# Optimization experiments

Measured on AMD Instinct MI355X. Metric: run time of the kernel, lower is better.

Reference implementation:

```python
import jax, jax.numpy as jnp
import numpy as np

B, H, W, NF = 2, 80, 80, 128  # batch, height, width, n_filter
CIN = 2 * NF                  # input channels (final conv outputs 2*NF and adds to x)


def _conv(x, w):
    # 3x3, stride 1, SAME, no bias; NHWC / HWIO
    return jax.lax.conv_general_dilated(
        x, w, window_strides=(1, 1), padding='SAME',
        dimension_numbers=('NHWC', 'HWIO', 'NHWC'))


def setup_inputs() -> dict:
    key = jax.random.key(0)
    ks = jax.random.split(key, 5)
    def glorot(k, shape):
        fan_in = shape[0] * shape[1] * shape[2]
        fan_out = shape[0] * shape[1] * shape[3]
        lim = np.sqrt(6.0 / (fan_in + fan_out)).astype(np.float32)
        return jax.random.uniform(k, shape, jnp.float32, -lim, lim)
    return {
        'x': jax.random.normal(ks[0], (B, H, W, CIN), jnp.float32),
        'w_theta': glorot(ks[1], (3, 3, CIN, NF)),
        'w_phi':   glorot(ks[2], (3, 3, CIN, NF)),
        'w_g':     glorot(ks[3], (3, 3, CIN, NF)),
        'w_conv':  glorot(ks[4], (3, 3, NF, CIN)),
    }


def reference(x, w_theta, w_phi, w_g, w_conv):
    b, h, w, cin = x.shape
    c = w_theta.shape[-1]  # n_filter
    n = h * w
    theta = _conv(x, w_theta).reshape(b, n, c)        # (B, N, C)
    # NOTE: Keras Reshape((n_filter,-1)) is a row-major reshape, NOT a transpose
    phi = _conv(x, w_phi).reshape(b, c, n)            # (B, C, N)
    attn = jax.nn.softmax(jnp.einsum('bnc,bcm->bnm', theta, phi), axis=-1)  # (B, N, N)
    g = _conv(x, w_g).reshape(b, n, c)                # (B, N, C)
    out = jnp.einsum('bnm,bmc->bnc', attn, g).reshape(b, h, w, c)
    out = _conv(out, w_conv)                          # (B, H, W, 2C)
    return x + out
```

## Files before the change

### kernel.cpp

```cpp
#include <hip/hip_runtime.h>
#include <hip/hip_bf16.h>

#define HH_ 80
#define WW_ 80
#define CIN_ 256
#define NF_ 128
#define NPIX_ 6400
#define NTOK_ 12800
#define NELEM_ (NTOK_ * NF_)
#define NXEL_  (NTOK_ * CIN_)
#define KW_    2304
#define KWC_   1152
#define WEL_   294912

#define KVS_    8
#define KVB_    32
#define MCHUNK_ 800
#define NIT_    25

__device__ float g_theta[NELEM_];
__device__ float g_phi  [NELEM_];
__device__ float g_gv   [NELEM_];
__device__ unsigned short g_aob[NELEM_];
__device__ unsigned short g_th_hi[NELEM_], g_th_lo[NELEM_];
__device__ unsigned short g_phT_hi[NELEM_], g_phT_lo[NELEM_];
__device__ unsigned short g_gT[NELEM_];
__device__ float g_po [KVS_ * NELEM_];
__device__ float g_pml[KVS_ * NTOK_ * 2];
__device__ unsigned short g_xh[NXEL_], g_xl[NXEL_];
__device__ unsigned short g_wtTh[WEL_], g_wtTl[WEL_];
__device__ unsigned short g_wpTh[WEL_], g_wpTl[WEL_];
__device__ unsigned short g_wgT[WEL_];
__device__ unsigned short g_wcT[WEL_];

__device__ __forceinline__ float b2f(unsigned short u) {
    union { unsigned int i; float f; } v; v.i = ((unsigned int)u) << 16; return v.f;
}
__device__ __forceinline__ unsigned short f2b(float f) {
    union { float f; unsigned int i; } v; v.f = f;
    unsigned int i = v.i;
    i += 0x7fffu + ((i >> 16) & 1u);
    return (unsigned short)(i >> 16);
}

typedef __attribute__((ext_vector_type(8))) short bf16x8;
typedef __attribute__((ext_vector_type(4))) float f32x4;

__device__ __forceinline__ f32x4 mfma16(bf16x8 a, bf16x8 b, f32x4 c) {
    return __builtin_amdgcn_mfma_f32_16x16x32_bf16(a, b, c, 0, 0, 0);
}

__global__ __launch_bounds__(256) void prep_x(const float* __restrict__ x)
{
    const int i = (blockIdx.x * 256 + threadIdx.x) * 4;
    if (i >= NXEL_) return;
    const float4 v = *(const float4*)(x + i);
    ushort4 hi, lo;
    hi.x = f2b(v.x); lo.x = f2b(v.x - b2f(hi.x));
    hi.y = f2b(v.y); lo.y = f2b(v.y - b2f(hi.y));
    hi.z = f2b(v.z); lo.z = f2b(v.z - b2f(hi.z));
    hi.w = f2b(v.w); lo.w = f2b(v.w - b2f(hi.w));
    *(ushort4*)(g_xh + i) = hi;
    *(ushort4*)(g_xl + i) = lo;
}

__global__ __launch_bounds__(256) void prep_w(
    const float* __restrict__ wt, const float* __restrict__ wp,
    const float* __restrict__ wg, const float* __restrict__ wc)
{
    const int i = blockIdx.x * 256 + threadIdx.x;
    if (i >= WEL_) return;
    {
        const int t  = i / (256 * 128);
        const int r  = i % (256 * 128);
        const int ci = r >> 7;
        const int f  = r & 127;
        const size_t d = (size_t)(t * 8 + (ci >> 5)) * 4096
                       + (size_t)f * 32 + (ci & 31);
        const float tv = wt[i];
        const unsigned short th = f2b(tv);
        g_wtTh[d] = th; g_wtTl[d] = f2b(tv - b2f(th));
        const float pv = wp[i];
        const unsigned short ph = f2b(pv);
        g_wpTh[d] = ph; g_wpTl[d] = f2b(pv - b2f(ph));
        g_wgT[d] = f2b(wg[i]);
    }
    {
        const int t  = i / (128 * 256);
        const int r  = i % (128 * 256);
        const int ci = r >> 8;
        const int f  = r & 255;
        const size_t d = (size_t)(t * 4 + (ci >> 5)) * 8192
                       + (size_t)f * 32 + (ci & 31);
        g_wcT[d] = f2b(wc[i]);
    }
}

__global__ __launch_bounds__(512) void conv3_mfma()
{
    __shared__ __align__(16) unsigned short w_lds[5][128][40];
    __shared__ __align__(16) unsigned short x_lds[64][2][40];

    const int tid  = threadIdx.x;
    const int wv   = tid >> 6;
    const int lane = tid & 63;
    const int quad = lane >> 4;
    const int ll   = lane & 15;
    const int wp   = wv >> 2;
    const int wf   = wv & 3;
    const int P0   = blockIdx.x * 64;
    const int fb   = wf * 32;

    const int sxp = tid >> 3;
    const int sxh = (tid >> 2) & 1;
    const int sxc = (tid & 3) * 8;
    const int swf = tid >> 2;
    const int swc = (tid & 3) * 8;

    const int sp  = P0 + sxp;
    const int spb = sp / NPIX_;
    const int spl = sp % NPIX_;
    const int sph = spl / WW_;
    const int spw = spl % WW_;

    const bf16x8 ZV = {0,0,0,0,0,0,0,0};
    bf16x8 rx, rw0, rw1, rw2, rw3, rw4;

#define C3_STAGE_LOAD(s)                                                      \
    {                                                                         \
        const int t_ = (s) >> 3, kc_ = (s) & 7;                               \
        const int hh_ = sph + t_ / 3 - 1, ww_ = spw + t_ % 3 - 1;             \
        if (hh_ >= 0 && hh_ < HH_ && ww_ >= 0 && ww_ < WW_) {                 \
            const size_t src_ = ((size_t)spb * NPIX_ + hh_ * WW_ + ww_) * CIN_\
                                + kc_ * 32 + sxc;                             \
            rx = sxh ? *(const bf16x8*)(g_xl + src_)                          \
                     : *(const bf16x8*)(g_xh + src_);                         \
        } else rx = ZV;                                                       \
        const size_t ws_ = (size_t)(s) * 4096 + (size_t)swf * 32 + swc;       \
        rw0 = *(const bf16x8*)(g_wtTh + ws_);                                 \
        rw1 = *(const bf16x8*)(g_wtTl + ws_);                                 \
        rw2 = *(const bf16x8*)(g_wpTh + ws_);                                 \
        rw3 = *(const bf16x8*)(g_wpTl + ws_);                                 \
        rw4 = *(const bf16x8*)(g_wgT  + ws_);                                 \
    }

#define C3_STAGE_WRITE()                                                      \
    {                                                                         \
        *(bf16x8*)(&x_lds[sxp][sxh][sxc]) = rx;                               \
        *(bf16x8*)(&w_lds[0][swf][swc]) = rw0;                                \
        *(bf16x8*)(&w_lds[1][swf][swc]) = rw1;                                \
        *(bf16x8*)(&w_lds[2][swf][swc]) = rw2;                                \
        *(bf16x8*)(&w_lds[3][swf][swc]) = rw3;                                \
        *(bf16x8*)(&w_lds[4][swf][swc]) = rw4;                                \
    }

    f32x4 aT[2][2], aP[2][2], aG[2][2];
    #pragma unroll
    for (int pt = 0; pt < 2; ++pt)
        #pragma unroll
        for (int ft = 0; ft < 2; ++ft) {
            aT[pt][ft] = (f32x4){0.f,0.f,0.f,0.f};
            aP[pt][ft] = (f32x4){0.f,0.f,0.f,0.f};
            aG[pt][ft] = (f32x4){0.f,0.f,0.f,0.f};
        }

    C3_STAGE_LOAD(0);
    C3_STAGE_WRITE();
    __syncthreads();

    for (int s = 0; s < 72; ++s) {
        const bool pf = (s + 1 < 72);
        if (pf) C3_STAGE_LOAD(s + 1);

        bf16x8 xa[2][2];
        #pragma unroll
        for (int pt = 0; pt < 2; ++pt) {
            const int px = wp * 32 + pt * 16 + ll;
            xa[pt][0] = *(const bf16x8*)(&x_lds[px][0][quad * 8]);
            xa[pt][1] = *(const bf16x8*)(&x_lds[px][1][quad * 8]);
        }
        #pragma unroll
        for (int ft = 0; ft < 2; ++ft) {
            const int f = fb + ft * 16 + ll;
            const bf16x8 tH = *(const bf16x8*)(&w_lds[0][f][quad * 8]);
            const bf16x8 tL = *(const bf16x8*)(&w_lds[1][f][quad * 8]);
            const bf16x8 pH = *(const bf16x8*)(&w_lds[2][f][quad * 8]);
            const bf16x8 pL = *(const bf16x8*)(&w_lds[3][f][quad * 8]);
            const bf16x8 gB = *(const bf16x8*)(&w_lds[4][f][quad * 8]);
            #pragma unroll
            for (int pt = 0; pt < 2; ++pt) {
                aT[pt][ft] = mfma16(xa[pt][0], tH, aT[pt][ft]);
                aT[pt][ft] = mfma16(xa[pt][0], tL, aT[pt][ft]);
                aT[pt][ft] = mfma16(xa[pt][1], tH, aT[pt][ft]);
                aP[pt][ft] = mfma16(xa[pt][0], pH, aP[pt][ft]);
                aP[pt][ft] = mfma16(xa[pt][0], pL, aP[pt][ft]);
                aP[pt][ft] = mfma16(xa[pt][1], pH, aP[pt][ft]);
                aG[pt][ft] = mfma16(xa[pt][0], gB, aG[pt][ft]);
            }
        }

        __syncthreads();
        if (pf) C3_STAGE_WRITE();
        __syncthreads();
    }

    #pragma unroll
    for (int pt = 0; pt < 2; ++pt)
        #pragma unroll
        for (int ft = 0; ft < 2; ++ft) {
            const int f = fb + ft * 16 + ll;
            #pragma unroll
            for (int r = 0; r < 4; ++r) {
                const size_t n = P0 + wp * 32 + pt * 16 + quad * 4 + r;
                g_theta[n * NF_ + f] = aT[pt][ft][r];
                g_phi  [n * NF_ + f] = aP[pt][ft][r];
                g_gv   [n * NF_ + f] = aG[pt][ft][r];
            }
        }
#undef C3_STAGE_LOAD
#undef C3_STAGE_WRITE
}

__global__ __launch_bounds__(256) void prep_pack()
{
    const int i = blockIdx.x * 256 + threadIdx.x;
    if (i >= NELEM_) return;
    const int n  = i >> 7;
    const int c  = i & 127;
    const int b  = n / NPIX_;
    const int nl = n % NPIX_;

    const float tv = g_theta[i];
    const unsigned short th = f2b(tv);
    g_th_hi[i] = th;
    g_th_lo[i] = f2b(tv - b2f(th));

    const float pv = g_phi[i];
    const int j  = nl * 128 + c;
    const int cp = j / NPIX_;
    const int mp = j % NPIX_;
    const unsigned short phh = f2b(pv);
    const size_t o = (size_t)b * (NPIX_ * NF_) + (size_t)mp * 128 + cp;
    g_phT_hi[o] = phh;
    g_phT_lo[o] = f2b(pv - b2f(phh));

    g_gT[(size_t)b * (NPIX_ * NF_) + (size_t)c * NPIX_ + nl] = f2b(g_gv[i]);
}

__global__ __launch_bounds__(256) void attn_mfma()
{
    __shared__ __align__(16) unsigned short kh_lds[KVB_][136];
    __shared__ __align__(16) unsigned short kl_lds[KVB_][136];
    __shared__ __align__(16) unsigned short v_lds[NF_][40];
    __shared__ __align__(16) short p_lds[4][16 * 40];

    const int tid  = threadIdx.x;
    const int w    = tid >> 6;
    const int lane = tid & 63;
    const int quad = lane >> 4;
    const int ll   = lane & 15;

    const int cid = blockIdx.x & 15;
    const int qw  = blockIdx.x >> 4;
    const int b   = cid >> 3;
    const int kvs = cid & 7;
    const int R0  = b * NPIX_ + qw * 64;
    const int m_start = kvs * MCHUNK_;

    const unsigned short* phH = g_phT_hi + (size_t)b * (NPIX_ * NF_);
    const unsigned short* phL = g_phT_lo + (size_t)b * (NPIX_ * NF_);
    const unsigned short* gT  = g_gT    + (size_t)b * (NPIX_ * NF_);

    bf16x8 aH[4], aL[4];
    #pragma unroll
    for (int kk = 0; kk < 4; ++kk) {
        const size_t off = (size_t)(R0 + w * 16 + ll) * 128 + kk * 32 + quad * 8;
        aH[kk] = *(const bf16x8*)(g_th_hi + off);
        aL[kk] = *(const bf16x8*)(g_th_lo + off);
    }

    f32x4 acc[8];
    #pragma unroll
    for (int t = 0; t < 8; ++t) acc[t] = (f32x4){0.f, 0.f, 0.f, 0.f};
    float mi = -1e30f, li = 0.f;

    const int kr0 = tid >> 4;
    const int kc0 = (tid & 15) * 8;
    const int vr0 = tid >> 2;
    const int vm0 = (tid & 3) * 8;

    bf16x8 skh0, skh1, skl0, skl1, sv0, sv1;

    {
        const int m0 = m_start;
        skh0 = *(const bf16x8*)(phH + (size_t)(m0 + kr0) * 128 + kc0);
        skh1 = *(const bf16x8*)(phH + (size_t)(m0 + kr0 + 16) * 128 + kc0);
        skl0 = *(const bf16x8*)(phL + (size_t)(m0 + kr0) * 128 + kc0);
        skl1 = *(const bf16x8*)(phL + (size_t)(m0 + kr0 + 16) * 128 + kc0);
        sv0  = *(const bf16x8*)(gT + (size_t)vr0 * NPIX_ + m0 + vm0);
        sv1  = *(const bf16x8*)(gT + (size_t)(vr0 + 64) * NPIX_ + m0 + vm0);
        *(bf16x8*)(&kh_lds[kr0][kc0])      = skh0;
        *(bf16x8*)(&kh_lds[kr0 + 16][kc0]) = skh1;
        *(bf16x8*)(&kl_lds[kr0][kc0])      = skl0;
        *(bf16x8*)(&kl_lds[kr0 + 16][kc0]) = skl1;
        *(bf16x8*)(&v_lds[vr0][vm0])       = sv0;
        *(bf16x8*)(&v_lds[vr0 + 64][vm0])  = sv1;
    }
    __syncthreads();

    short* pl = &p_lds[w][0];

    for (int it = 0; it < NIT_; ++it) {
        const bool pf = (it + 1 < NIT_);
        if (pf) {
            const int m0 = m_start + (it + 1) * KVB_;
            skh0 = *(const bf16x8*)(phH + (size_t)(m0 + kr0) * 128 + kc0);
            skh1 = *(const bf16x8*)(phH + (size_t)(m0 + kr0 + 16) * 128 + kc0);
            skl0 = *(const bf16x8*)(phL + (size_t)(m0 + kr0) * 128 + kc0);
            skl1 = *(const bf16x8*)(phL + (size_t)(m0 + kr0 + 16) * 128 + kc0);
            sv0  = *(const bf16x8*)(gT + (size_t)vr0 * NPIX_ + m0 + vm0);
            sv1  = *(const bf16x8*)(gT + (size_t)(vr0 + 64) * NPIX_ + m0 + vm0);
        }

        f32x4 s[2];
        #pragma unroll
        for (int mt = 0; mt < 2; ++mt) {
            f32x4 s0 = (f32x4){0.f,0.f,0.f,0.f};
            const int mrow = mt * 16 + ll;
            #pragma unroll
            for (int kk = 0; kk < 4; ++kk) {
                const bf16x8 bH = *(const bf16x8*)(&kh_lds[mrow][kk * 32 + quad * 8]);
                const bf16x8 bL = *(const bf16x8*)(&kl_lds[mrow][kk * 32 + quad * 8]);
                s0 = mfma16(bH, aH[kk], s0);
                s0 = mfma16(bL, aH[kk], s0);
                s0 = mfma16(bH, aL[kk], s0);
            }
            s[mt] = s0;
        }

        float cm = fmaxf(fmaxf(fmaxf(s[0][0], s[0][1]), fmaxf(s[0][2], s[0][3])),
                         fmaxf(fmaxf(s[1][0], s[1][1]), fmaxf(s[1][2], s[1][3])));
        cm = fmaxf(cm, __shfl_xor(cm, 16));
        cm = fmaxf(cm, __shfl_xor(cm, 32));
        const bool nog = __all(cm <= mi + 4.0f);
        if (!nog) {
            const float nm = fmaxf(mi, cm);
            const float al = __expf(mi - nm);
            mi = nm;
            li *= al;
            if (quad == 0)
                ((float*)(pl + (ll >> 2) * 40 + 32))[ll & 3] = al;
        }
        float ssum = 0.f;
        #pragma unroll
        for (int mt = 0; mt < 2; ++mt)
            #pragma unroll
            for (int r = 0; r < 4; ++r) {
                const float e = __expf(s[mt][r] - mi);
                s[mt][r] = e; ssum += e;
            }
        ssum += __shfl_xor(ssum, 16);
        ssum += __shfl_xor(ssum, 32);
        li += ssum;

        #pragma unroll
        for (int mt = 0; mt < 2; ++mt) {
            unsigned int c0_, c1_;
            asm("v_cvt_pk_bf16_f32 %0, %1, %2"
                : "=v"(c0_) : "v"(s[mt][0]), "v"(s[mt][1]));
            asm("v_cvt_pk_bf16_f32 %0, %1, %2"
                : "=v"(c1_) : "v"(s[mt][2]), "v"(s[mt][3]));
            *(uint2*)(pl + ll * 40 + mt * 16 + quad * 4) = make_uint2(c0_, c1_);
        }

        if (!nog) {
            const float* alp = (const float*)(pl + quad * 40 + 32);
            #pragma unroll
            for (int r = 0; r < 4; ++r) {
                const float av = alp[r];
                #pragma unroll
                for (int t = 0; t < 8; ++t) acc[t][r] *= av;
            }
        }

        const bf16x8 pa = *(const bf16x8*)(pl + ll * 40 + quad * 8);

        #pragma unroll
        for (int ct = 0; ct < 8; ++ct) {
            const bf16x8 gb = *(const bf16x8*)(&v_lds[ct * 16 + ll][quad * 8]);
            acc[ct] = mfma16(pa, gb, acc[ct]);
        }

        __syncthreads();
        if (pf) {
            *(bf16x8*)(&kh_lds[kr0][kc0])      = skh0;
            *(bf16x8*)(&kh_lds[kr0 + 16][kc0]) = skh1;
            *(bf16x8*)(&kl_lds[kr0][kc0])      = skl0;
            *(bf16x8*)(&kl_lds[kr0 + 16][kc0]) = skl1;
            *(bf16x8*)(&v_lds[vr0][vm0])       = sv0;
            *(bf16x8*)(&v_lds[vr0 + 64][vm0])  = sv1;
        }
        __syncthreads();
    }

    const int row0 = R0 + w * 16;
    #pragma unroll
    for (int ct = 0; ct < 8; ++ct)
        #pragma unroll
        for (int r = 0; r < 4; ++r)
            g_po[((size_t)kvs * NTOK_ + row0 + quad * 4 + r) * NF_ + ct * 16 + ll]
                = acc[ct][r];
    if (quad == 0) {
        const size_t mlidx = ((size_t)kvs * NTOK_ + row0 + ll) * 2;
        g_pml[mlidx]     = mi;
        g_pml[mlidx + 1] = li;
    }
}

__global__ __launch_bounds__(256) void merge_attn()
{
    const int idx = blockIdx.x * 256 + threadIdx.x;
    const int row = idx >> 4;
    const int c0  = (idx & 15) * 8;

    float m[KVS_], l[KVS_];
    #pragma unroll
    for (int s = 0; s < KVS_; ++s) {
        const size_t mlidx = ((size_t)s * NTOK_ + row) * 2;
        m[s] = g_pml[mlidx];
        l[s] = g_pml[mlidx + 1];
    }
    float M = m[0];
    #pragma unroll
    for (int s = 1; s < KVS_; ++s) M = fmaxf(M, m[s]);
    float a[KVS_], L = 0.f;
    #pragma unroll
    for (int s = 0; s < KVS_; ++s) {
        a[s] = __expf(m[s] - M);
        L += a[s] * l[s];
    }
    const float inv = 1.f / L;

    float o[8];
    #pragma unroll
    for (int j = 0; j < 8; ++j) o[j] = 0.f;
    #pragma unroll
    for (int s = 0; s < KVS_; ++s) {
        const float* p = g_po + ((size_t)s * NTOK_ + row) * NF_ + c0;
        const float4 p0 = *(const float4*)(p);
        const float4 p1 = *(const float4*)(p + 4);
        o[0] += a[s] * p0.x; o[1] += a[s] * p0.y;
        o[2] += a[s] * p0.z; o[3] += a[s] * p0.w;
        o[4] += a[s] * p1.x; o[5] += a[s] * p1.y;
        o[6] += a[s] * p1.z; o[7] += a[s] * p1.w;
    }
    unsigned short tmp[8];
    #pragma unroll
    for (int j = 0; j < 8; ++j) tmp[j] = f2b(o[j] * inv);
    unsigned short* dst = g_aob + (size_t)row * NF_ + c0;
    *(ushort4*)(dst)     = make_ushort4(tmp[0], tmp[1], tmp[2], tmp[3]);
    *(ushort4*)(dst + 4) = make_ushort4(tmp[4], tmp[5], tmp[6], tmp[7]);
}

__global__ __launch_bounds__(512) void conv_out_mfma(
    const float* __restrict__ x, float* __restrict__ out)
{
    __shared__ __align__(16) unsigned short w_lds[256][40];
    __shared__ __align__(16) unsigned short a_lds[64][40];

    const int tid  = threadIdx.x;
    const int wv   = tid >> 6;
    const int lane = tid & 63;
    const int quad = lane >> 4;
    const int ll   = lane & 15;
    const int wp   = wv >> 2;
    const int wf   = wv & 3;
    const int P0   = blockIdx.x * 64;
    const int fb   = wf * 64;

    const int swf = tid >> 1;
    const int swc = (tid & 1) * 16;
    const int sap = tid >> 2;
    const int sac = (tid & 3) * 8;

    const int sp  = P0 + sap;
    const int spb = sp / NPIX_;
    const int spl = sp % NPIX_;
    const int sph = spl / WW_;
    const int spw = spl % WW_;

    const bf16x8 ZV = {0,0,0,0,0,0,0,0};
    bf16x8 ra, rwA, rwB;

#define CO_STAGE_LOAD(s)                                                      \
    {                                                                         \
        const int t_ = (s) >> 2, kc_ = (s) & 3;                               \
        if (tid < 256) {                                                      \
            const int hh_ = sph + t_ / 3 - 1, ww_ = spw + t_ % 3 - 1;         \
            if (hh_ >= 0 && hh_ < HH_ && ww_ >= 0 && ww_ < WW_) {             \
                const size_t src_ = ((size_t)spb * NPIX_ + hh_ * WW_ + ww_)   \
                                    * NF_ + kc_ * 32 + sac;                   \
                ra = *(const bf16x8*)(g_aob + src_);                          \
            } else ra = ZV;                                                   \
        }                                                                     \
        const size_t ws_ = (size_t)(s) * 8192 + (size_t)swf * 32 + swc;       \
        rwA = *(const bf16x8*)(g_wcT + ws_);                                  \
        rwB = *(const bf16x8*)(g_wcT + ws_ + 8);                              \
    }

#define CO_STAGE_WRITE()                                                      \
    {                                                                         \
        if (tid < 256) *(bf16x8*)(&a_lds[sap][sac]) = ra;                     \
        *(bf16x8*)(&w_lds[swf][swc])     = rwA;                               \
        *(bf16x8*)(&w_lds[swf][swc + 8]) = rwB;                               \
    }

    f32x4 acc[2][4];
    #pragma unroll
    for (int pt = 0; pt < 2; ++pt)
        #pragma unroll
        for (int ft = 0; ft < 4; ++ft) acc[pt][ft] = (f32x4){0.f,0.f,0.f,0.f};

    CO_STAGE_LOAD(0);
    CO_STAGE_WRITE();
    __syncthreads();

    for (int s = 0; s < 36; ++s) {
        const bool pf = (s + 1 < 36);
        if (pf) CO_STAGE_LOAD(s + 1);

        bf16x8 a[2];
        #pragma unroll
        for (int pt = 0; pt < 2; ++pt)
            a[pt] = *(const bf16x8*)(&a_lds[wp * 32 + pt * 16 + ll][quad * 8]);
        #pragma unroll
        for (int ft = 0; ft < 4; ++ft) {
            const bf16x8 bw = *(const bf16x8*)(&w_lds[fb + ft * 16 + ll][quad * 8]);
            #pragma unroll
            for (int pt = 0; pt < 2; ++pt)
                acc[pt][ft] = mfma16(a[pt], bw, acc[pt][ft]);
        }

        __syncthreads();
        if (pf) CO_STAGE_WRITE();
        __syncthreads();
    }

    #pragma unroll
    for (int pt = 0; pt < 2; ++pt)
        #pragma unroll
        for (int ft = 0; ft < 4; ++ft) {
            const int f = fb + ft * 16 + ll;
            #pragma unroll
            for (int r = 0; r < 4; ++r) {
                const size_t n = P0 + wp * 32 + pt * 16 + quad * 4 + r;
                const size_t oi = n * CIN_ + f;
                out[oi] = x[oi] + acc[pt][ft][r];
            }
        }
#undef CO_STAGE_LOAD
#undef CO_STAGE_WRITE
}

extern "C" void kernel_launch(void* const* d_in, const int* in_sizes, int n_in,
                              void* d_out, int out_size, void* d_ws, size_t ws_size,
                              hipStream_t stream)
{
    const float* x  = (const float*)d_in[0];
    const float* wt = (const float*)d_in[1];
    const float* wp = (const float*)d_in[2];
    const float* wg = (const float*)d_in[3];
    const float* wc = (const float*)d_in[4];
    float* out = (float*)d_out;

    prep_x<<<NXEL_ / 4 / 256, 256, 0, stream>>>(x);
    prep_w<<<(WEL_ + 255) / 256, 256, 0, stream>>>(wt, wp, wg, wc);
    conv3_mfma<<<NTOK_ / 64, 512, 0, stream>>>();
    prep_pack<<<(NELEM_ + 255) / 256, 256, 0, stream>>>();
    attn_mfma<<<(NTOK_ / 64) * KVS_, 256, 0, stream>>>();
    merge_attn<<<NTOK_ * 16 / 256, 256, 0, stream>>>();
    conv_out_mfma<<<NTOK_ / 64, 512, 0, stream>>>(x, out);
}
```

Before: 376.0 us.

## Switch attention to 32x32x16 MFMA with 32 query rows per wave

The attention kernel now gives each wave 32 query rows and uses 32x32x16 bf16 MFMAs for both the score and PV products, so each block covers 128 queries. Every K/V tile loaded into LDS is reused across twice as many queries, which halves the block count and the total K/V traffic. The online-softmax rescale factors move to a dedicated LDS array. In exchange, accumulator register use rises (four f32x16 plus eight-deep theta fragments), which can lower occupancy, and the grid shrinks to 800 blocks.

```diff
diff --git a/kernel.cpp b/kernel.cpp
--- a/kernel.cpp
+++ b/kernel.cpp
@@ -45,9 +45,13 @@
 
 typedef __attribute__((ext_vector_type(8))) short bf16x8;
 typedef __attribute__((ext_vector_type(4))) float f32x4;
+typedef __attribute__((ext_vector_type(16))) float f32x16;
 
 __device__ __forceinline__ f32x4 mfma16(bf16x8 a, bf16x8 b, f32x4 c) {
     return __builtin_amdgcn_mfma_f32_16x16x32_bf16(a, b, c, 0, 0, 0);
+}
+__device__ __forceinline__ f32x16 mfma32(bf16x8 a, bf16x8 b, f32x16 c) {
+    return __builtin_amdgcn_mfma_f32_32x32x16_bf16(a, b, c, 0, 0, 0);
 }
 
 __global__ __launch_bounds__(256) void prep_x(const float* __restrict__ x)
@@ -252,36 +256,39 @@
     __shared__ __align__(16) unsigned short kh_lds[KVB_][136];
     __shared__ __align__(16) unsigned short kl_lds[KVB_][136];
     __shared__ __align__(16) unsigned short v_lds[NF_][40];
-    __shared__ __align__(16) short p_lds[4][16 * 40];
+    __shared__ __align__(16) short p_lds[4][32 * 40];
+    __shared__ float al_lds[4][32];
 
     const int tid  = threadIdx.x;
     const int w    = tid >> 6;
     const int lane = tid & 63;
-    const int quad = lane >> 4;
-    const int ll   = lane & 15;
+    const int l31  = lane & 31;
+    const int lh   = lane >> 5;
 
     const int cid = blockIdx.x & 15;
     const int qw  = blockIdx.x >> 4;
     const int b   = cid >> 3;
     const int kvs = cid & 7;
-    const int R0  = b * NPIX_ + qw * 64;
+    const int R0  = b * NPIX_ + qw * 128;
     const int m_start = kvs * MCHUNK_;
 
     const unsigned short* phH = g_phT_hi + (size_t)b * (NPIX_ * NF_);
     const unsigned short* phL = g_phT_lo + (size_t)b * (NPIX_ * NF_);
     const unsigned short* gT  = g_gT    + (size_t)b * (NPIX_ * NF_);
 
-    bf16x8 aH[4], aL[4];
-    #pragma unroll
-    for (int kk = 0; kk < 4; ++kk) {
-        const size_t off = (size_t)(R0 + w * 16 + ll) * 128 + kk * 32 + quad * 8;
-        aH[kk] = *(const bf16x8*)(g_th_hi + off);
-        aL[kk] = *(const bf16x8*)(g_th_lo + off);
-    }
-
-    f32x4 acc[8];
-    #pragma unroll
-    for (int t = 0; t < 8; ++t) acc[t] = (f32x4){0.f, 0.f, 0.f, 0.f};
+    bf16x8 tHf[8], tLf[8];
+    #pragma unroll
+    for (int kk = 0; kk < 8; ++kk) {
+        const size_t off = (size_t)(R0 + w * 32 + l31) * 128 + kk * 16 + lh * 8;
+        tHf[kk] = *(const bf16x8*)(g_th_hi + off);
+        tLf[kk] = *(const bf16x8*)(g_th_lo + off);
+    }
+
+    f32x16 acc[4];
+    #pragma unroll
+    for (int ct = 0; ct < 4; ++ct)
+        #pragma unroll
+        for (int i = 0; i < 16; ++i) acc[ct][i] = 0.f;
     float mi = -1e30f, li = 0.f;
 
     const int kr0 = tid >> 4;
@@ -322,25 +329,21 @@
             sv1  = *(const bf16x8*)(gT + (size_t)(vr0 + 64) * NPIX_ + m0 + vm0);
         }
 
-        f32x4 s[2];
-        #pragma unroll
-        for (int mt = 0; mt < 2; ++mt) {
-            f32x4 s0 = (f32x4){0.f,0.f,0.f,0.f};
-            const int mrow = mt * 16 + ll;
-            #pragma unroll
-            for (int kk = 0; kk < 4; ++kk) {
-                const bf16x8 bH = *(const bf16x8*)(&kh_lds[mrow][kk * 32 + quad * 8]);
-                const bf16x8 bL = *(const bf16x8*)(&kl_lds[mrow][kk * 32 + quad * 8]);
-                s0 = mfma16(bH, aH[kk], s0);
-                s0 = mfma16(bL, aH[kk], s0);
-                s0 = mfma16(bH, aL[kk], s0);
-            }
-            s[mt] = s0;
-        }
-
-        float cm = fmaxf(fmaxf(fmaxf(s[0][0], s[0][1]), fmaxf(s[0][2], s[0][3])),
-                         fmaxf(fmaxf(s[1][0], s[1][1]), fmaxf(s[1][2], s[1][3])));
-        cm = fmaxf(cm, __shfl_xor(cm, 16));
+        f32x16 s;
+        #pragma unroll
+        for (int i = 0; i < 16; ++i) s[i] = 0.f;
+        #pragma unroll
+        for (int kk = 0; kk < 8; ++kk) {
+            const bf16x8 kH = *(const bf16x8*)(&kh_lds[l31][kk * 16 + lh * 8]);
+            const bf16x8 kL = *(const bf16x8*)(&kl_lds[l31][kk * 16 + lh * 8]);
+            s = mfma32(kH, tHf[kk], s);
+            s = mfma32(kL, tHf[kk], s);
+            s = mfma32(kH, tLf[kk], s);
+        }
+
+        float cm = s[0];
+        #pragma unroll
+        for (int i = 1; i < 16; ++i) cm = fmaxf(cm, s[i]);
         cm = fmaxf(cm, __shfl_xor(cm, 32));
         const bool nog = __all(cm <= mi + 4.0f);
         if (!nog) {
@@ -348,47 +351,49 @@
             const float al = __expf(mi - nm);
             mi = nm;
             li *= al;
-            if (quad == 0)
-                ((float*)(pl + (ll >> 2) * 40 + 32))[ll & 3] = al;
+            if (lh == 0) al_lds[w][l31] = al;
         }
         float ssum = 0.f;
         #pragma unroll
-        for (int mt = 0; mt < 2; ++mt)
-            #pragma unroll
-            for (int r = 0; r < 4; ++r) {
-                const float e = __expf(s[mt][r] - mi);
-                s[mt][r] = e; ssum += e;
-            }
-        ssum += __shfl_xor(ssum, 16);
+        for (int i = 0; i < 16; ++i) {
+            const float e = __expf(s[i] - mi);
+            s[i] = e; ssum += e;
+        }
         ssum += __shfl_xor(ssum, 32);
         li += ssum;
 
         #pragma unroll
-        for (int mt = 0; mt < 2; ++mt) {
+        for (int rg = 0; rg < 4; ++rg) {
             unsigned int c0_, c1_;
             asm("v_cvt_pk_bf16_f32 %0, %1, %2"
-                : "=v"(c0_) : "v"(s[mt][0]), "v"(s[mt][1]));
+                : "=v"(c0_) : "v"(s[rg * 4 + 0]), "v"(s[rg * 4 + 1]));
             asm("v_cvt_pk_bf16_f32 %0, %1, %2"
-                : "=v"(c1_) : "v"(s[mt][2]), "v"(s[mt][3]));
-            *(uint2*)(pl + ll * 40 + mt * 16 + quad * 4) = make_uint2(c0_, c1_);
+                : "=v"(c1_) : "v"(s[rg * 4 + 2]), "v"(s[rg * 4 + 3]));
+            *(uint2*)(pl + l31 * 40 + rg * 8 + lh * 4) = make_uint2(c0_, c1_);
         }
 
         if (!nog) {
-            const float* alp = (const float*)(pl + quad * 40 + 32);
             #pragma unroll
-            for (int r = 0; r < 4; ++r) {
-                const float av = alp[r];
+            for (int rg = 0; rg < 4; ++rg) {
+                const float4 a4 = *(const float4*)(&al_lds[w][rg * 8 + lh * 4]);
                 #pragma unroll
-                for (int t = 0; t < 8; ++t) acc[t][r] *= av;
+                for (int ct = 0; ct < 4; ++ct) {
+                    acc[ct][rg * 4 + 0] *= a4.x;
+                    acc[ct][rg * 4 + 1] *= a4.y;
+                    acc[ct][rg * 4 + 2] *= a4.z;
+                    acc[ct][rg * 4 + 3] *= a4.w;
+                }
             }
         }
 
-        const bf16x8 pa = *(const bf16x8*)(pl + ll * 40 + quad * 8);
-
-        #pragma unroll
-        for (int ct = 0; ct < 8; ++ct) {
-            const bf16x8 gb = *(const bf16x8*)(&v_lds[ct * 16 + ll][quad * 8]);
-            acc[ct] = mfma16(pa, gb, acc[ct]);
+        const bf16x8 pa0 = *(const bf16x8*)(pl + l31 * 40 + 0  + lh * 8);
+        const bf16x8 pa1 = *(const bf16x8*)(pl + l31 * 40 + 16 + lh * 8);
+        #pragma unroll
+        for (int ct = 0; ct < 4; ++ct) {
+            const bf16x8 gb0 = *(const bf16x8*)(&v_lds[ct * 32 + l31][0  + lh * 8]);
+            const bf16x8 gb1 = *(const bf16x8*)(&v_lds[ct * 32 + l31][16 + lh * 8]);
+            acc[ct] = mfma32(pa0, gb0, acc[ct]);
+            acc[ct] = mfma32(pa1, gb1, acc[ct]);
         }
 
         __syncthreads();
@@ -403,15 +408,17 @@
         __syncthreads();
     }
 
-    const int row0 = R0 + w * 16;
-    #pragma unroll
-    for (int ct = 0; ct < 8; ++ct)
-        #pragma unroll
-        for (int r = 0; r < 4; ++r)
-            g_po[((size_t)kvs * NTOK_ + row0 + quad * 4 + r) * NF_ + ct * 16 + ll]
-                = acc[ct][r];
-    if (quad == 0) {
-        const size_t mlidx = ((size_t)kvs * NTOK_ + row0 + ll) * 2;
+    const int row0 = R0 + w * 32;
+    #pragma unroll
+    for (int ct = 0; ct < 4; ++ct)
+        #pragma unroll
+        for (int i = 0; i < 16; ++i) {
+            const int q = (i & 3) + 8 * (i >> 2) + 4 * lh;
+            g_po[((size_t)kvs * NTOK_ + row0 + q) * NF_ + ct * 32 + l31]
+                = acc[ct][i];
+        }
+    if (lh == 0) {
+        const size_t mlidx = ((size_t)kvs * NTOK_ + row0 + l31) * 2;
         g_pml[mlidx]     = mi;
         g_pml[mlidx + 1] = li;
     }
@@ -577,7 +584,7 @@
     prep_w<<<(WEL_ + 255) / 256, 256, 0, stream>>>(wt, wp, wg, wc);
     conv3_mfma<<<NTOK_ / 64, 512, 0, stream>>>();
     prep_pack<<<(NELEM_ + 255) / 256, 256, 0, stream>>>();
-    attn_mfma<<<(NTOK_ / 64) * KVS_, 256, 0, stream>>>();
+    attn_mfma<<<(NTOK_ / 128) * KVS_, 256, 0, stream>>>();
     merge_attn<<<NTOK_ * 16 / 256, 256, 0, stream>>>();
     conv_out_mfma<<<NTOK_ / 64, 512, 0, stream>>>(x, out);
 }
```

Result: slower. 411.7 us (+9.5%).
